# Performance work log

Measured on AMD Instinct MI355X. Metric: run time of the kernel, lower is better.

## Reference

```python
import jax, jax.numpy as jnp
import numpy as np

D_MODEL = 768
NUM_HEADS = 12
HEAD_DIM = D_MODEL // NUM_HEADS


def setup_inputs() -> dict:
    key = jax.random.key(0)
    ks = jax.random.split(key, 12)
    B, S = 4, 1024
    x = jax.random.normal(ks[0], (B, S, D_MODEL), dtype=jnp.float32)
    boxes = jax.random.uniform(ks[1], (B, S, 4), dtype=jnp.float32)
    s = 1.0 / np.sqrt(D_MODEL)
    Wq = jax.random.normal(ks[2], (D_MODEL, D_MODEL), dtype=jnp.float32) * s
    bq = jnp.zeros((D_MODEL,), dtype=jnp.float32)
    Wk = jax.random.normal(ks[3], (D_MODEL, D_MODEL), dtype=jnp.float32) * s
    bk = jnp.zeros((D_MODEL,), dtype=jnp.float32)
    Wv = jax.random.normal(ks[4], (D_MODEL, D_MODEL), dtype=jnp.float32) * s
    bv = jnp.zeros((D_MODEL,), dtype=jnp.float32)
    Wo = jax.random.normal(ks[5], (D_MODEL, D_MODEL), dtype=jnp.float32) * s
    bo = jnp.zeros((D_MODEL,), dtype=jnp.float32)
    spatial_bias = jax.random.normal(ks[6], (NUM_HEADS,), dtype=jnp.float32)
    return {"x": x, "boxes": boxes, "Wq": Wq, "bq": bq, "Wk": Wk, "bk": bk,
            "Wv": Wv, "bv": bv, "Wo": Wo, "bo": bo, "spatial_bias": spatial_bias}


def reference(x, boxes, Wq, bq, Wk, bk, Wv, bv, Wo, bo, spatial_bias):
    B, S, _ = x.shape
    H, Dh = NUM_HEADS, HEAD_DIM
    # projections -> [B, H, S, Dh]
    def proj(W, b):
        return (x @ W.T + b).reshape(B, S, H, Dh).transpose(0, 2, 1, 3)
    Q, K, V = proj(Wq, bq), proj(Wk, bk), proj(Wv, bv)
    scores = jnp.einsum('bhsd,bhtd->bhst', Q, K) / np.sqrt(Dh)
    # spatial bias from box-center pairwise distances
    centers = jnp.stack([(boxes[:, :, 0] + boxes[:, :, 2]) * 0.5,
                         (boxes[:, :, 1] + boxes[:, :, 3]) * 0.5], axis=-1)  # [B,S,2]
    diff = centers[:, :, None, :] - centers[:, None, :, :]                    # [B,S,S,2]
    dist = jnp.linalg.norm(diff, axis=-1)                                     # [B,S,S]
    bias = -dist[:, None, :, :] * spatial_bias[None, :, None, None]           # [B,H,S,S]
    attn = jax.nn.softmax(scores + bias, axis=-1)
    attended = jnp.einsum('bhst,bhtd->bhsd', attn, V)
    attended = attended.transpose(0, 2, 1, 3).reshape(B, S, H * Dh)
    return attended @ Wo.T + bo
```

## Files before the change

kernel.cpp:

```cpp
#include <hip/hip_runtime.h>
#include <hip/hip_bf16.h>
#include <stdint.h>

#define NHEADS 12
#define HDIM   64
#define NB     4
#define SQ     1024
#define DM     768
#define NROWS  (NB*SQ)
#define NWE    (DM*DM)
#define NXE    (NROWS*DM)

typedef __attribute__((ext_vector_type(8))) short short8;
typedef __attribute__((ext_vector_type(4))) float f32x4;

__device__ __forceinline__ unsigned short f2bf(float f) {
  union { float f; unsigned u; } v; v.f = f;
  return (unsigned short)((v.u + 0x7fffu + ((v.u >> 16) & 1u)) >> 16);
}

__device__ __forceinline__ unsigned pkbf(float lo, float hi) {
  __hip_bfloat162 h;
  h.x = __float2bfloat16(lo);
  h.y = __float2bfloat16(hi);
  return *reinterpret_cast<unsigned*>(&h);
}

__device__ __forceinline__ void gload16(const void* g, void* l) {
  __builtin_amdgcn_global_load_lds((__attribute__((address_space(1))) void*)(void*)g,
                                   (__attribute__((address_space(3))) void*)l, 16, 0, 0);
}

__device__ __forceinline__ void drain_dma() {
  asm volatile("s_waitcnt vmcnt(0)" ::: "memory");
  __builtin_amdgcn_sched_barrier(0);
}

__global__ __launch_bounds__(256) void prep_kernel(
    const float* __restrict__ x, const float* __restrict__ Wq, const float* __restrict__ Wk,
    const float* __restrict__ Wv, const float* __restrict__ Wo, const float* __restrict__ boxes,
    unsigned short* __restrict__ xb, unsigned short* __restrict__ wcat,
    unsigned short* __restrict__ wob, float2* __restrict__ centers) {
  int i = blockIdx.x * 256 + threadIdx.x;
  if (i < NXE) { xb[i] = f2bf(x[i]); return; }
  i -= NXE;
  if (i < NWE) {
    wcat[i]           = f2bf(Wq[i]);
    wcat[NWE + i]     = f2bf(Wk[i]);
    wcat[2 * NWE + i] = f2bf(Wv[i]);
    wob[i]            = f2bf(Wo[i]);
    return;
  }
  i -= NWE;
  if (i < NROWS) {
    float4 bx = ((const float4*)boxes)[i];
    centers[i] = make_float2((bx.x + bx.z) * 0.5f, (bx.y + bx.w) * 0.5f);
  }
}

template <int EPI, int BM, int BN>
__global__ __launch_bounds__(256, 2) void gemm_bt(
    const unsigned short* __restrict__ A, const unsigned short* __restrict__ Bw,
    int K, int tiles_n,
    const float* __restrict__ b0, const float* __restrict__ b1, const float* __restrict__ b2,
    unsigned short* __restrict__ outQ, unsigned short* __restrict__ outK,
    unsigned short* __restrict__ outVt, float* __restrict__ outF) {
  constexpr int MF = BM / 32, NF = BN / 32;
  __shared__ unsigned short lA[2][BM * 32];
  __shared__ unsigned short lB[2][BN * 32];
  const int tid = threadIdx.x, wave = tid >> 6, lane = tid & 63;
  const int tm = blockIdx.x / tiles_n, tn = blockIdx.x % tiles_n;
  const int wr = wave >> 1, wc = wave & 1;
  const int g = lane >> 4, c16 = lane & 15, kb8 = g * 8;

  f32x4 acc[MF][NF];
#pragma unroll
  for (int m = 0; m < MF; m++)
#pragma unroll
    for (int n = 0; n < NF; n++) acc[m][n] = (f32x4){0.f, 0.f, 0.f, 0.f};

  const unsigned short* Abase = A + (size_t)tm * BM * K;
  const unsigned short* Bbase = Bw + (size_t)tn * BN * K;
  const int srow = lane >> 2, scb = (lane & 3) << 4;

  auto stage = [&](int kt, int s) {
#pragma unroll
    for (int c = wave; c < BM / 16; c += 4)
      gload16((const char*)(Abase + (size_t)(c * 16 + srow) * K + kt) + scb,
              (char*)lA[s] + c * 1024);
#pragma unroll
    for (int c = wave; c < BN / 16; c += 4)
      gload16((const char*)(Bbase + (size_t)(c * 16 + srow) * K + kt) + scb,
              (char*)lB[s] + c * 1024);
  };

  stage(0, 0);
  const int nk = K >> 5;
#pragma unroll 1
  for (int i = 0; i < nk; i++) {
    drain_dma();
    __syncthreads();
    if (i + 1 < nk) stage((i + 1) * 32, (i + 1) & 1);
    const unsigned short* sA = lA[i & 1];
    const unsigned short* sB = lB[i & 1];
    short8 a[MF], b[NF];
#pragma unroll
    for (int m = 0; m < MF; m++)
      a[m] = *(const short8*)&sA[(wr * (BM / 2) + m * 16 + c16) * 32 + kb8];
#pragma unroll
    for (int n = 0; n < NF; n++)
      b[n] = *(const short8*)&sB[(wc * (BN / 2) + n * 16 + c16) * 32 + kb8];
#pragma unroll
    for (int m = 0; m < MF; m++)
#pragma unroll
      for (int n = 0; n < NF; n++)
        acc[m][n] = __builtin_amdgcn_mfma_f32_16x16x32_bf16(a[m], b[n], acc[m][n], 0, 0, 0);
  }

#pragma unroll
  for (int m = 0; m < MF; m++) {
    const int gm0 = tm * BM + wr * (BM / 2) + m * 16 + g * 4;
    const int bb = gm0 >> 10, ss0 = gm0 & 1023;
#pragma unroll
    for (int n = 0; n < NF; n++) {
      const int gn = tn * BN + wc * (BN / 2) + n * 16 + c16;
      if (EPI == 0) {
        const int which = gn / DM, nn = gn - which * DM;
        const int h = nn >> 6, dh = nn & 63;
        const float bias = (which == 0 ? b0 : which == 1 ? b1 : b2)[nn];
        const float scale = (which == 0) ? 0.1803368801f : 1.0f;
        if (which == 2) {
          ushort4 pk;
          pk.x = f2bf(acc[m][n][0] + bias);
          pk.y = f2bf(acc[m][n][1] + bias);
          pk.z = f2bf(acc[m][n][2] + bias);
          pk.w = f2bf(acc[m][n][3] + bias);
          *(ushort4*)&outVt[(((size_t)bb * NHEADS + h) * HDIM + dh) * SQ + ss0] = pk;
        } else {
          unsigned short* dst = (which == 0 ? outQ : outK) + ((size_t)bb * NHEADS + h) * SQ * HDIM;
#pragma unroll
          for (int r = 0; r < 4; r++)
            dst[(size_t)(ss0 + r) * HDIM + dh] = f2bf((acc[m][n][r] + bias) * scale);
        }
      } else {
        const float bias = b0[gn];
#pragma unroll
        for (int r = 0; r < 4; r++)
          outF[(size_t)(gm0 + r) * DM + gn] = acc[m][n][r] + bias;
      }
    }
  }
}

#define KVB 64
#define NT  (SQ / KVB)
__global__ __launch_bounds__(256, 3) void attn_kernel(
    const unsigned short* __restrict__ Qb, const unsigned short* __restrict__ Kb,
    const unsigned short* __restrict__ Vt, const float2* __restrict__ centers,
    const float* __restrict__ sbias, unsigned short* __restrict__ attb) {
  __shared__ unsigned short lK[2][KVB * HDIM];
  __shared__ unsigned short lV[2][HDIM * KVB];
  __shared__ unsigned short plds[4][16 * KVB];
  __shared__ float2 cent_s[SQ];
  const int tid = threadIdx.x, wave = tid >> 6, lane = tid & 63;
  const int g = lane >> 4, c16 = lane & 15, kb8 = g * 8;
  const int bid = blockIdx.x;
  const int xcd = bid & 7, li = bid >> 3;
  const int bh = xcd * 6 + (li >> 4);
  const int qt = li & 15;
  const int b = bh / NHEADS, h = bh - b * NHEADS;
  const float sb = sbias[h] * 1.44269504f;

  const unsigned short* Qh = Qb + (size_t)bh * SQ * HDIM;
  const char* Kc = (const char*)(Kb + (size_t)bh * SQ * HDIM);
  const char* Vc = (const char*)(Vt + (size_t)bh * HDIM * SQ);

  for (int i = tid; i < SQ; i += 256) cent_s[i] = centers[b * SQ + i];
  __syncthreads();

  auto stage = [&](int tbn, int s) {
#pragma unroll
    for (int j = 0; j < 2; j++) {
      const int c = wave * 2 + j;
      gload16(Kc + (size_t)(tbn + lane) * 128 + c * 16, (char*)lK[s] + c * 1024);
      gload16(Vc + (size_t)lane * 2048 + (size_t)(tbn + c * 8) * 2, (char*)lV[s] + c * 1024);
    }
  };

  const int q = qt * 64 + wave * 16 + c16;
  short8 qf[2];
  qf[0] = *(const short8*)&Qh[(size_t)q * HDIM + kb8];
  qf[1] = *(const short8*)&Qh[(size_t)q * HDIM + 32 + kb8];
  const float2 cq = cent_s[q];

  float mreg = -1e30f, lreg = 0.f;
  f32x4 oacc[4];
#pragma unroll
  for (int dd = 0; dd < 4; dd++) oacc[dd] = (f32x4){0.f, 0.f, 0.f, 0.f};

  stage(0, 0);
#pragma unroll 1
  for (int t = 0; t < NT; t++) {
    const int cur = t & 1;
    drain_dma();
    __syncthreads();
    if (t + 1 < NT) stage((t + 1) * KVB, cur ^ 1);
    const char* K0 = (const char*)lK[cur];
    const char* V0 = (const char*)lV[cur];
    const int tb = t * KVB;
    f32x4 sv[4];
#pragma unroll
    for (int cc = 0; cc < 4; cc++) {
      short8 k0 = *(const short8*)(K0 + g * 1024 + (cc * 16 + c16) * 16);
      short8 k1 = *(const short8*)(K0 + (4 + g) * 1024 + (cc * 16 + c16) * 16);
      f32x4 s = (f32x4){0.f, 0.f, 0.f, 0.f};
      s = __builtin_amdgcn_mfma_f32_16x16x32_bf16(k0, qf[0], s, 0, 0, 0);
      s = __builtin_amdgcn_mfma_f32_16x16x32_bf16(k1, qf[1], s, 0, 0, 0);
      sv[cc] = s;
    }
#pragma unroll
    for (int cc = 0; cc < 4; cc++) {
      const float4* cp = (const float4*)&cent_s[tb + cc * 16 + g * 4];
      float4 c01 = cp[0], c23 = cp[1];
      float dx, dy;
      dx = cq.x - c01.x; dy = cq.y - c01.y;
      sv[cc][0] -= __builtin_amdgcn_sqrtf(dx * dx + dy * dy) * sb;
      dx = cq.x - c01.z; dy = cq.y - c01.w;
      sv[cc][1] -= __builtin_amdgcn_sqrtf(dx * dx + dy * dy) * sb;
      dx = cq.x - c23.x; dy = cq.y - c23.y;
      sv[cc][2] -= __builtin_amdgcn_sqrtf(dx * dx + dy * dy) * sb;
      dx = cq.x - c23.z; dy = cq.y - c23.w;
      sv[cc][3] -= __builtin_amdgcn_sqrtf(dx * dx + dy * dy) * sb;
    }
    float lm = -1e30f;
#pragma unroll
    for (int cc = 0; cc < 4; cc++) {
      float a0 = fmaxf(sv[cc][0], sv[cc][1]), a1 = fmaxf(sv[cc][2], sv[cc][3]);
      lm = fmaxf(lm, fmaxf(a0, a1));
    }
    if (!__all(lm <= mreg + 8.0f)) {
      float vmax = fmaxf(lm, __shfl_xor(lm, 16));
      vmax = fmaxf(vmax, __shfl_xor(vmax, 32));
      const float mn = fmaxf(mreg, vmax);
      const float sc = __builtin_amdgcn_exp2f(mreg - mn);
      lreg *= sc;
#pragma unroll
      for (int dd = 0; dd < 4; dd++)
#pragma unroll
        for (int r = 0; r < 4; r++) oacc[dd][r] *= sc;
      mreg = mn;
    }
    float ps = 0.f;
#pragma unroll
    for (int cc = 0; cc < 4; cc++)
#pragma unroll
      for (int r = 0; r < 4; r++) {
        sv[cc][r] = __builtin_amdgcn_exp2f(sv[cc][r] - mreg);
        ps += sv[cc][r];
      }
    lreg += ps;
    char* P0 = (char*)&plds[wave][0];
#pragma unroll
    for (int cc = 0; cc < 4; cc++) {
      uint2 u;
      u.x = pkbf(sv[cc][0], sv[cc][1]);
      u.y = pkbf(sv[cc][2], sv[cc][3]);
      *(uint2*)(P0 + (cc * 2 + (g >> 1)) * 256 + c16 * 16 + (g & 1) * 8) = u;
    }
#pragma unroll
    for (int kc = 0; kc < 2; kc++) {
      short8 pf = *(const short8*)(P0 + (kc * 4 + g) * 256 + c16 * 16);
#pragma unroll
      for (int dd = 0; dd < 4; dd++) {
        short8 vf = *(const short8*)(V0 + (kc * 4 + g) * 1024 + (dd * 16 + c16) * 16);
        oacc[dd] = __builtin_amdgcn_mfma_f32_16x16x32_bf16(vf, pf, oacc[dd], 0, 0, 0);
      }
    }
  }
  lreg += __shfl_xor(lreg, 16);
  lreg += __shfl_xor(lreg, 32);
  const float inv = 1.f / lreg;
#pragma unroll
  for (int dd = 0; dd < 4; dd++) {
    uint2 u;
    u.x = pkbf(oacc[dd][0] * inv, oacc[dd][1] * inv);
    u.y = pkbf(oacc[dd][2] * inv, oacc[dd][3] * inv);
    *(uint2*)&attb[(size_t)(b * SQ + q) * DM + h * HDIM + dd * 16 + g * 4] = u;
  }
}

extern "C" void kernel_launch(void* const* d_in, const int* in_sizes, int n_in,
                              void* d_out, int out_size, void* d_ws, size_t ws_size,
                              hipStream_t stream) {
  const float* x     = (const float*)d_in[0];
  const float* boxes = (const float*)d_in[1];
  const float* Wq    = (const float*)d_in[2];
  const float* bq    = (const float*)d_in[3];
  const float* Wk    = (const float*)d_in[4];
  const float* bk    = (const float*)d_in[5];
  const float* Wv    = (const float*)d_in[6];
  const float* bv    = (const float*)d_in[7];
  const float* Wo    = (const float*)d_in[8];
  const float* bo    = (const float*)d_in[9];
  const float* sb    = (const float*)d_in[10];

  char* ws = (char*)d_ws;
  unsigned short* xb   = (unsigned short*)(ws);
  unsigned short* wcat = (unsigned short*)(ws + 6291456);
  unsigned short* wob  = (unsigned short*)(ws + 9830400);
  unsigned short* qb   = (unsigned short*)(ws + 11010048);
  unsigned short* kb   = (unsigned short*)(ws + 17301504);
  unsigned short* vtb  = (unsigned short*)(ws + 23592960);
  unsigned short* attb = (unsigned short*)(ws + 29884416);
  float2* centers      = (float2*)(ws + 36175872);
  float* out = (float*)d_out;

  prep_kernel<<<14608, 256, 0, stream>>>(x, Wq, Wk, Wv, Wo, boxes, xb, wcat, wob, centers);
  gemm_bt<0, 128, 96><<<32 * 24, 256, 0, stream>>>(xb, wcat, DM, 24, bq, bk, bv,
                                                   qb, kb, vtb, nullptr);
  attn_kernel<<<768, 256, 0, stream>>>(qb, kb, vtb, centers, sb, attb);
  gemm_bt<1, 64, 64><<<64 * 12, 256, 0, stream>>>(attb, wob, DM, 12, bo, nullptr, nullptr,
                                                  nullptr, nullptr, nullptr, out);
}
```

Baseline: 93.13 us.

## Software-pipeline QK^T of next tile with softmax/PV of current tile

Restructures the attention loop so that the QK^T MFMAs and spatial-bias computation for tile t+1 are issued after the softmax and PV for tile t. This lets matrix work overlap with the exp/sqrt vector work. K gets triple buffering and V keeps double buffering, with separate staging for each. The loop is unrolled by two so the score registers alternate between two sets. Box centers are now read straight from global memory instead of being staged in LDS, which frees LDS and drops a prologue sync but puts global loads inside the inner loop.

Result: slower. 99.34 us (+6.7%).

```diff
diff --git a/kernel.cpp b/kernel.cpp
--- a/kernel.cpp
+++ b/kernel.cpp
@@ -154,14 +154,95 @@
 
 #define KVB 64
 #define NT  (SQ / KVB)
+#define KBUF 8192
+
+#define QKT_BIAS(SVN, ko, tb2)                                                 \
+  {                                                                            \
+    const char* Kp = (const char*)lK + (ko);                                   \
+    _Pragma("unroll")                                                          \
+    for (int cc = 0; cc < 4; cc++) {                                           \
+      short8 k0 = *(const short8*)(Kp + g * 1024 + (cc * 16 + c16) * 16);      \
+      short8 k1 = *(const short8*)(Kp + (4 + g) * 1024 + (cc * 16 + c16) * 16);\
+      f32x4 s = (f32x4){0.f, 0.f, 0.f, 0.f};                                   \
+      s = __builtin_amdgcn_mfma_f32_16x16x32_bf16(k0, qf[0], s, 0, 0, 0);      \
+      s = __builtin_amdgcn_mfma_f32_16x16x32_bf16(k1, qf[1], s, 0, 0, 0);      \
+      SVN[cc] = s;                                                             \
+    }                                                                          \
+    _Pragma("unroll")                                                          \
+    for (int cc = 0; cc < 4; cc++) {                                           \
+      const float4* cp = (const float4*)&cent_g[(tb2) + cc * 16 + g * 4];      \
+      float4 c01 = cp[0], c23 = cp[1];                                         \
+      float dx, dy;                                                            \
+      dx = cq.x - c01.x; dy = cq.y - c01.y;                                    \
+      SVN[cc][0] -= __builtin_amdgcn_sqrtf(dx * dx + dy * dy) * sb;            \
+      dx = cq.x - c01.z; dy = cq.y - c01.w;                                    \
+      SVN[cc][1] -= __builtin_amdgcn_sqrtf(dx * dx + dy * dy) * sb;            \
+      dx = cq.x - c23.x; dy = cq.y - c23.y;                                    \
+      SVN[cc][2] -= __builtin_amdgcn_sqrtf(dx * dx + dy * dy) * sb;            \
+      dx = cq.x - c23.z; dy = cq.y - c23.w;                                    \
+      SVN[cc][3] -= __builtin_amdgcn_sqrtf(dx * dx + dy * dy) * sb;            \
+    }                                                                          \
+  }
+
+#define SOFTMAX_PV(SVC, vo)                                                    \
+  {                                                                            \
+    float lm = -1e30f;                                                         \
+    _Pragma("unroll")                                                          \
+    for (int cc = 0; cc < 4; cc++) {                                           \
+      float a0 = fmaxf(SVC[cc][0], SVC[cc][1]);                                \
+      float a1 = fmaxf(SVC[cc][2], SVC[cc][3]);                                \
+      lm = fmaxf(lm, fmaxf(a0, a1));                                           \
+    }                                                                          \
+    if (!__all(lm <= mreg + 8.0f)) {                                           \
+      float vmax = fmaxf(lm, __shfl_xor(lm, 16));                              \
+      vmax = fmaxf(vmax, __shfl_xor(vmax, 32));                                \
+      const float mn = fmaxf(mreg, vmax);                                      \
+      const float sc = __builtin_amdgcn_exp2f(mreg - mn);                      \
+      lreg *= sc;                                                              \
+      _Pragma("unroll")                                                        \
+      for (int dd = 0; dd < 4; dd++)                                           \
+        _Pragma("unroll")                                                      \
+        for (int r = 0; r < 4; r++) oacc[dd][r] *= sc;                         \
+      mreg = mn;                                                               \
+    }                                                                          \
+    float ps = 0.f;                                                            \
+    _Pragma("unroll")                                                          \
+    for (int cc = 0; cc < 4; cc++)                                             \
+      _Pragma("unroll")                                                        \
+      for (int r = 0; r < 4; r++) {                                            \
+        SVC[cc][r] = __builtin_amdgcn_exp2f(SVC[cc][r] - mreg);                \
+        ps += SVC[cc][r];                                                      \
+      }                                                                        \
+    lreg += ps;                                                                \
+    char* P0 = (char*)&plds[wave][0];                                          \
+    _Pragma("unroll")                                                          \
+    for (int cc = 0; cc < 4; cc++) {                                           \
+      uint2 u;                                                                 \
+      u.x = pkbf(SVC[cc][0], SVC[cc][1]);                                      \
+      u.y = pkbf(SVC[cc][2], SVC[cc][3]);                                      \
+      *(uint2*)(P0 + (cc * 2 + (g >> 1)) * 256 + c16 * 16 + (g & 1) * 8) = u;  \
+    }                                                                          \
+    const char* V0 = (const char*)lV + (vo);                                   \
+    _Pragma("unroll")                                                          \
+    for (int kc = 0; kc < 2; kc++) {                                           \
+      short8 pf = *(const short8*)(P0 + (kc * 4 + g) * 256 + c16 * 16);        \
+      _Pragma("unroll")                                                        \
+      for (int dd = 0; dd < 4; dd++) {                                         \
+        short8 vf = *(const short8*)(V0 + (kc * 4 + g) * 1024 +                \
+                                     (dd * 16 + c16) * 16);                    \
+        oacc[dd] = __builtin_amdgcn_mfma_f32_16x16x32_bf16(vf, pf, oacc[dd],   \
+                                                           0, 0, 0);           \
+      }                                                                        \
+    }                                                                          \
+  }
+
 __global__ __launch_bounds__(256, 3) void attn_kernel(
     const unsigned short* __restrict__ Qb, const unsigned short* __restrict__ Kb,
     const unsigned short* __restrict__ Vt, const float2* __restrict__ centers,
     const float* __restrict__ sbias, unsigned short* __restrict__ attb) {
-  __shared__ unsigned short lK[2][KVB * HDIM];
-  __shared__ unsigned short lV[2][HDIM * KVB];
+  __shared__ unsigned short lK[3 * KVB * HDIM];
+  __shared__ unsigned short lV[2 * HDIM * KVB];
   __shared__ unsigned short plds[4][16 * KVB];
-  __shared__ float2 cent_s[SQ];
   const int tid = threadIdx.x, wave = tid >> 6, lane = tid & 63;
   const int g = lane >> 4, c16 = lane & 15, kb8 = g * 8;
   const int bid = blockIdx.x;
@@ -174,16 +255,20 @@
   const unsigned short* Qh = Qb + (size_t)bh * SQ * HDIM;
   const char* Kc = (const char*)(Kb + (size_t)bh * SQ * HDIM);
   const char* Vc = (const char*)(Vt + (size_t)bh * HDIM * SQ);
-
-  for (int i = tid; i < SQ; i += 256) cent_s[i] = centers[b * SQ + i];
-  __syncthreads();
-
-  auto stage = [&](int tbn, int s) {
+  const float2* cent_g = centers + b * SQ;
+
+  auto stageK = [&](int tbn, int bo) {
 #pragma unroll
     for (int j = 0; j < 2; j++) {
       const int c = wave * 2 + j;
-      gload16(Kc + (size_t)(tbn + lane) * 128 + c * 16, (char*)lK[s] + c * 1024);
-      gload16(Vc + (size_t)lane * 2048 + (size_t)(tbn + c * 8) * 2, (char*)lV[s] + c * 1024);
+      gload16(Kc + (size_t)(tbn + lane) * 128 + c * 16, (char*)lK + bo + c * 1024);
+    }
+  };
+  auto stageV = [&](int tbn, int bo) {
+#pragma unroll
+    for (int j = 0; j < 2; j++) {
+      const int c = wave * 2 + j;
+      gload16(Vc + (size_t)lane * 2048 + (size_t)(tbn + c * 8) * 2, (char*)lV + bo + c * 1024);
     }
   };
 
@@ -191,90 +276,42 @@
   short8 qf[2];
   qf[0] = *(const short8*)&Qh[(size_t)q * HDIM + kb8];
   qf[1] = *(const short8*)&Qh[(size_t)q * HDIM + 32 + kb8];
-  const float2 cq = cent_s[q];
+  const float2 cq = cent_g[q];
 
   float mreg = -1e30f, lreg = 0.f;
   f32x4 oacc[4];
 #pragma unroll
   for (int dd = 0; dd < 4; dd++) oacc[dd] = (f32x4){0.f, 0.f, 0.f, 0.f};
 
-  stage(0, 0);
+  stageK(0, 0);
+  stageK(KVB, KBUF);
+  stageV(0, 0);
+  drain_dma();
+  __syncthreads();
+  f32x4 svA[4], svB[4];
+  QKT_BIAS(svA, 0, 0);
+
 #pragma unroll 1
-  for (int t = 0; t < NT; t++) {
-    const int cur = t & 1;
-    drain_dma();
-    __syncthreads();
-    if (t + 1 < NT) stage((t + 1) * KVB, cur ^ 1);
-    const char* K0 = (const char*)lK[cur];
-    const char* V0 = (const char*)lV[cur];
-    const int tb = t * KVB;
-    f32x4 sv[4];
-#pragma unroll
-    for (int cc = 0; cc < 4; cc++) {
-      short8 k0 = *(const short8*)(K0 + g * 1024 + (cc * 16 + c16) * 16);
-      short8 k1 = *(const short8*)(K0 + (4 + g) * 1024 + (cc * 16 + c16) * 16);
-      f32x4 s = (f32x4){0.f, 0.f, 0.f, 0.f};
-      s = __builtin_amdgcn_mfma_f32_16x16x32_bf16(k0, qf[0], s, 0, 0, 0);
-      s = __builtin_amdgcn_mfma_f32_16x16x32_bf16(k1, qf[1], s, 0, 0, 0);
-      sv[cc] = s;
-    }
-#pragma unroll
-    for (int cc = 0; cc < 4; cc++) {
-      const float4* cp = (const float4*)&cent_s[tb + cc * 16 + g * 4];
-      float4 c01 = cp[0], c23 = cp[1];
-      float dx, dy;
-      dx = cq.x - c01.x; dy = cq.y - c01.y;
-      sv[cc][0] -= __builtin_amdgcn_sqrtf(dx * dx + dy * dy) * sb;
-      dx = cq.x - c01.z; dy = cq.y - c01.w;
-      sv[cc][1] -= __builtin_amdgcn_sqrtf(dx * dx + dy * dy) * sb;
-      dx = cq.x - c23.x; dy = cq.y - c23.y;
-      sv[cc][2] -= __builtin_amdgcn_sqrtf(dx * dx + dy * dy) * sb;
-      dx = cq.x - c23.z; dy = cq.y - c23.w;
-      sv[cc][3] -= __builtin_amdgcn_sqrtf(dx * dx + dy * dy) * sb;
-    }
-    float lm = -1e30f;
-#pragma unroll
-    for (int cc = 0; cc < 4; cc++) {
-      float a0 = fmaxf(sv[cc][0], sv[cc][1]), a1 = fmaxf(sv[cc][2], sv[cc][3]);
-      lm = fmaxf(lm, fmaxf(a0, a1));
-    }
-    if (!__all(lm <= mreg + 8.0f)) {
-      float vmax = fmaxf(lm, __shfl_xor(lm, 16));
-      vmax = fmaxf(vmax, __shfl_xor(vmax, 32));
-      const float mn = fmaxf(mreg, vmax);
-      const float sc = __builtin_amdgcn_exp2f(mreg - mn);
-      lreg *= sc;
-#pragma unroll
-      for (int dd = 0; dd < 4; dd++)
-#pragma unroll
-        for (int r = 0; r < 4; r++) oacc[dd][r] *= sc;
-      mreg = mn;
-    }
-    float ps = 0.f;
-#pragma unroll
-    for (int cc = 0; cc < 4; cc++)
-#pragma unroll
-      for (int r = 0; r < 4; r++) {
-        sv[cc][r] = __builtin_amdgcn_exp2f(sv[cc][r] - mreg);
-        ps += sv[cc][r];
+  for (int i = 0; i < 8; i++) {
+    {
+      const int t = 2 * i;
+      drain_dma();
+      __syncthreads();
+      stageV((t + 1) * KVB, ((t + 1) & 1) * KBUF);
+      if (i < 7) stageK((t + 2) * KVB, ((t + 2) % 3) * KBUF);
+      SOFTMAX_PV(svA, (t & 1) * KBUF);
+      QKT_BIAS(svB, ((t + 1) % 3) * KBUF, (t + 1) * KVB);
+    }
+    {
+      const int t = 2 * i + 1;
+      drain_dma();
+      __syncthreads();
+      if (i < 7) {
+        stageV((t + 1) * KVB, ((t + 1) & 1) * KBUF);
+        stageK((t + 2) * KVB, ((t + 2) % 3) * KBUF);
       }
-    lreg += ps;
-    char* P0 = (char*)&plds[wave][0];
-#pragma unroll
-    for (int cc = 0; cc < 4; cc++) {
-      uint2 u;
-      u.x = pkbf(sv[cc][0], sv[cc][1]);
-      u.y = pkbf(sv[cc][2], sv[cc][3]);
-      *(uint2*)(P0 + (cc * 2 + (g >> 1)) * 256 + c16 * 16 + (g & 1) * 8) = u;
-    }
-#pragma unroll
-    for (int kc = 0; kc < 2; kc++) {
-      short8 pf = *(const short8*)(P0 + (kc * 4 + g) * 256 + c16 * 16);
-#pragma unroll
-      for (int dd = 0; dd < 4; dd++) {
-        short8 vf = *(const short8*)(V0 + (kc * 4 + g) * 1024 + (dd * 16 + c16) * 16);
-        oacc[dd] = __builtin_amdgcn_mfma_f32_16x16x32_bf16(vf, pf, oacc[dd], 0, 0, 0);
-      }
+      SOFTMAX_PV(svB, (t & 1) * KBUF);
+      if (i < 7) QKT_BIAS(svA, ((t + 1) % 3) * KBUF, (t + 1) * KVB);
     }
   }
   lreg += __shfl_xor(lreg, 16);
```
